# Kernel optimization log

Hardware: AMD Instinct MI355X
Metric: run time of the kernel (lower is better)

Reference implementation:

```python
import jax, jax.numpy as jnp
import numpy as np

RES = 128          # voxel grid resolution
N = 262144
C_IN = 64
C_OUT = 64
K = 3              # kernel size -> 27 offsets


def _build_rulebook(coords, res, k):
    """Submanifold sparse conv rulebook (stride=1, padding=k//2).
    Returns in_idx, out_idx [K^3, N] int32 and mask [K^3, N] float32."""
    n = coords.shape[0]
    lin = (coords[:, 0] * res + coords[:, 1]) * res + coords[:, 2]
    order = np.argsort(lin)
    sorted_lin = lin[order]
    r = k // 2
    in_idx, out_idx, mask = [], [], []
    for dx in range(-r, r + 1):
        for dy in range(-r, r + 1):
            for dz in range(-r, r + 1):
                nb = coords + np.array([dx, dy, dz])
                inb = np.all((nb >= 0) & (nb < res), axis=1)
                nlin = (nb[:, 0] * res + nb[:, 1]) * res + nb[:, 2]
                pos = np.searchsorted(sorted_lin, nlin)
                pos_c = np.clip(pos, 0, n - 1)
                found = inb & (sorted_lin[pos_c] == nlin)
                in_idx.append(np.where(found, order[pos_c], 0))
                out_idx.append(np.where(found, np.arange(n), 0))
                mask.append(found.astype(np.float32))
    return (np.asarray(in_idx, np.int32), np.asarray(out_idx, np.int32),
            np.asarray(mask, np.float32))


def setup_inputs() -> dict:
    rng = np.random.default_rng(0)
    lin = rng.choice(RES ** 3, size=N, replace=False)
    coords = np.stack([lin // (RES * RES), (lin // RES) % RES, lin % RES], axis=1)
    in_idx, out_idx, mask = _build_rulebook(coords, RES, K)

    key = jax.random.key(0)
    kf, kw, kb = jax.random.split(key, 3)
    feats = jax.random.normal(kf, (N, C_IN), dtype=jnp.float32)
    weight = jax.random.normal(kw, (K ** 3, C_IN, C_OUT), dtype=jnp.float32) * 0.02
    bias = jax.random.normal(kb, (C_OUT,), dtype=jnp.float32) * 0.02
    return {
        "feats": feats,
        "weight": weight,
        "bias": bias,
        "in_idx": jnp.asarray(in_idx),
        "out_idx": jnp.asarray(out_idx),
        "mask": jnp.asarray(mask),
    }


def reference(feats, weight, bias, in_idx, out_idx, mask):
    # gather -> GEMM -> scatter per kernel offset (27 fixed offsets)
    n = feats.shape[0]
    out = jnp.tile(bias[None, :], (n, 1))  # [N, C_out]
    for k in range(weight.shape[0]):
        g = feats[in_idx[k]] * mask[k][:, None]   # [N, C_in], zeros where no pair
        out = out.at[out_idx[k]].add(g @ weight[k])  # invalid rows add zeros at row 0
    return out
```

## Files before the change

kernel.cpp:

```cpp
#include <hip/hip_runtime.h>

#define CIN  64
#define COUT 64
#define KVOL 27

typedef __attribute__((ext_vector_type(8))) short bf16x8;
typedef __attribute__((ext_vector_type(4))) float f32x4;

union U4H8 { uint4 u; bf16x8 h; };

static __device__ __forceinline__ unsigned short f2bf(float x) {
    union { float f; unsigned int u; } v; v.f = x;
    return (unsigned short)((v.u + 0x7FFFu + ((v.u >> 16) & 1u)) >> 16);
}

__global__ __launch_bounds__(256) void pack_w(const float* __restrict__ W,
                                              unsigned short* __restrict__ wf) {
    int t = blockIdx.x * 256 + threadIdx.x;
    if (t >= KVOL * 8 * 64) return;
    int lane  = t & 63;
    int frag  = (t >> 6) & 7;
    int k     = t >> 9;
    int kh    = frag >> 2, nt = frag & 3;
    int col   = nt * 16 + (lane & 15);
    int kbase = kh * 32 + (lane >> 4) * 8;
    const float* src = W + (size_t)k * (CIN * COUT) + (size_t)kbase * COUT + col;
    unsigned int pk[4];
    #pragma unroll
    for (int j = 0; j < 4; ++j) {
        unsigned int lo = f2bf(src[(2 * j) * COUT]);
        unsigned int hi = f2bf(src[(2 * j + 1) * COUT]);
        pk[j] = lo | (hi << 16);
    }
    *reinterpret_cast<uint4*>(wf + (size_t)t * 8) = make_uint4(pk[0], pk[1], pk[2], pk[3]);
}

__global__ __launch_bounds__(256) void cvt_feats(const float* __restrict__ f,
                                                 uint4* __restrict__ o, int total8) {
    int t = blockIdx.x * 256 + threadIdx.x;
    if (t < total8) {
        const float4* p = reinterpret_cast<const float4*>(f) + 2 * (size_t)t;
        float4 a = p[0], b = p[1];
        unsigned int u0 = (unsigned int)f2bf(a.x) | ((unsigned int)f2bf(a.y) << 16);
        unsigned int u1 = (unsigned int)f2bf(a.z) | ((unsigned int)f2bf(a.w) << 16);
        unsigned int u2 = (unsigned int)f2bf(b.x) | ((unsigned int)f2bf(b.y) << 16);
        unsigned int u3 = (unsigned int)f2bf(b.z) | ((unsigned int)f2bf(b.w) << 16);
        o[t] = make_uint4(u0, u1, u2, u3);
    } else if (t < total8 + 8) {
        o[t] = make_uint4(0u, 0u, 0u, 0u);
    }
}

__global__ __launch_bounds__(256) void spconv_mfma64(
    const char* __restrict__ fbf,
    const uint4* __restrict__ wf4,
    const float* __restrict__ bias,
    const int*   __restrict__ in_idx,
    const float* __restrict__ mask,
    float* __restrict__ out, int n)
{
    const int tid  = threadIdx.x;
    const int lane = tid & 63;
    const int wv   = tid >> 6;
    const int rloc = lane & 15;
    const int grp  = lane >> 4;

    const int nwg = gridDim.x;
    int bid = blockIdx.x;
    if ((nwg & 7) == 0) {
        const int chunk = nwg >> 3;
        bid = (blockIdx.x & 7) * chunk + (blockIdx.x >> 3);
    }
    const int row0 = bid * 256 + wv * 64;

    __shared__ uint4 lds_w[2][512];

    f32x4 acc[4][4];
    #pragma unroll
    for (int nt = 0; nt < 4; ++nt) {
        float b = bias[nt * 16 + rloc];
        f32x4 v = {b, b, b, b};
        acc[0][nt] = v; acc[1][nt] = v; acc[2][nt] = v; acc[3][nt] = v;
    }

    int rowt[4];
    #pragma unroll
    for (int t = 0; t < 4; ++t) rowt[t] = row0 + 16 * t + rloc;

    const unsigned zoff = (unsigned)n * 128u;

    lds_w[0][tid]       = wf4[tid];
    lds_w[0][tid + 256] = wf4[tid + 256];
    __syncthreads();

    U4H8 a[3][4][2];
    {
        int i0[4]; float m0[4];
        #pragma unroll
        for (int t = 0; t < 4; ++t) { i0[t] = in_idx[rowt[t]]; m0[t] = mask[rowt[t]]; }
        #pragma unroll
        for (int t = 0; t < 4; ++t) {
            unsigned o = (m0[t] != 0.0f) ? (unsigned)i0[t] * 128u : zoff;
            const uint4* p = reinterpret_cast<const uint4*>(fbf + o) + grp;
            a[0][t][0].u = p[0];
            a[0][t][1].u = p[4];
        }
        #pragma unroll
        for (int t = 0; t < 4; ++t) { i0[t] = in_idx[(size_t)n + rowt[t]]; m0[t] = mask[(size_t)n + rowt[t]]; }
        #pragma unroll
        for (int t = 0; t < 4; ++t) {
            unsigned o = (m0[t] != 0.0f) ? (unsigned)i0[t] * 128u : zoff;
            const uint4* p = reinterpret_cast<const uint4*>(fbf + o) + grp;
            a[1][t][0].u = p[0];
            a[1][t][1].u = p[4];
        }
    }

    int idxb[2][4]; float mskb[2][4];
    #pragma unroll
    for (int t = 0; t < 4; ++t) {
        idxb[0][t] = in_idx[(size_t)2 * n + rowt[t]];
        mskb[0][t] = mask[(size_t)2 * n + rowt[t]];
    }
    #pragma unroll
    for (int t = 0; t < 4; ++t) {
        idxb[1][t] = in_idx[(size_t)3 * n + rowt[t]];
        mskb[1][t] = mask[(size_t)3 * n + rowt[t]];
    }

    #pragma unroll
    for (int k = 0; k < KVOL; ++k) {
        const int cur  = k & 1;
        const int nxt  = cur ^ 1;
        const int cslot = k % 3;
        const int gslot = (k + 2) % 3;
        const int islot = k & 1;

        uint4 w0, w1;
        if (k + 1 < KVOL) {
            const uint4* s = wf4 + (size_t)(k + 1) * 512;
            w0 = s[tid]; w1 = s[tid + 256];
        }

        if (k + 2 < KVOL) {
            #pragma unroll
            for (int t = 0; t < 4; ++t) {
                unsigned o = (mskb[islot][t] != 0.0f) ? (unsigned)idxb[islot][t] * 128u : zoff;
                const uint4* p = reinterpret_cast<const uint4*>(fbf + o) + grp;
                a[gslot][t][0].u = p[0];
                a[gslot][t][1].u = p[4];
            }
        }

        if (k + 4 < KVOL) {
            const size_t kb = (size_t)(k + 4) * n;
            #pragma unroll
            for (int t = 0; t < 4; ++t) {
                idxb[islot][t] = in_idx[kb + rowt[t]];
                mskb[islot][t] = mask[kb + rowt[t]];
            }
        }

        __builtin_amdgcn_sched_barrier(0);

        U4H8 bf[2][4];
        #pragma unroll
        for (int kh = 0; kh < 2; ++kh)
            #pragma unroll
            for (int ntl = 0; ntl < 4; ++ntl)
                bf[kh][ntl].u = lds_w[cur][(kh * 4 + ntl) * 64 + lane];

        #pragma unroll
        for (int t = 0; t < 4; ++t)
            #pragma unroll
            for (int ntl = 0; ntl < 4; ++ntl) {
                acc[t][ntl] = __builtin_amdgcn_mfma_f32_16x16x32_bf16(a[cslot][t][0].h, bf[0][ntl].h, acc[t][ntl], 0, 0, 0);
                acc[t][ntl] = __builtin_amdgcn_mfma_f32_16x16x32_bf16(a[cslot][t][1].h, bf[1][ntl].h, acc[t][ntl], 0, 0, 0);
            }

        if (k + 1 < KVOL) {
            lds_w[nxt][tid]       = w0;
            lds_w[nxt][tid + 256] = w1;
            asm volatile("s_waitcnt lgkmcnt(0)" ::: "memory");
            __builtin_amdgcn_s_barrier();
        }
    }

    #pragma unroll
    for (int t = 0; t < 4; ++t)
        #pragma unroll
        for (int ntl = 0; ntl < 4; ++ntl)
            #pragma unroll
            for (int r = 0; r < 4; ++r) {
                int orow = row0 + 16 * t + grp * 4 + r;
                out[(size_t)orow * COUT + ntl * 16 + rloc] = acc[t][ntl][r];
            }
}

static __device__ __forceinline__ bf16x8 cvt8(float4 a, float4 b, float m) {
    bf16x8 r;
    r[0] = (short)f2bf(a.x * m); r[1] = (short)f2bf(a.y * m);
    r[2] = (short)f2bf(a.z * m); r[3] = (short)f2bf(a.w * m);
    r[4] = (short)f2bf(b.x * m); r[5] = (short)f2bf(b.y * m);
    r[6] = (short)f2bf(b.z * m); r[7] = (short)f2bf(b.w * m);
    return r;
}

__global__ __launch_bounds__(256) void spconv_mfma_f32(
    const float* __restrict__ feats,
    const unsigned short* __restrict__ wf,
    const float* __restrict__ bias,
    const int*   __restrict__ in_idx,
    const float* __restrict__ mask,
    float* __restrict__ out, int n)
{
    const int tid  = threadIdx.x;
    const int lane = tid & 63;
    const int wv   = tid >> 6;
    const int rloc = lane & 15;
    const int grp  = lane >> 4;
    const int row0 = blockIdx.x * 128 + wv * 32;

    __shared__ uint4 lds_w[2][512];

    f32x4 acc[2][4];
    #pragma unroll
    for (int nt = 0; nt < 4; ++nt) {
        float b = bias[nt * 16 + rloc];
        f32x4 v = {b, b, b, b};
        acc[0][nt] = v; acc[1][nt] = v;
    }

    const uint4* wf4 = reinterpret_cast<const uint4*>(wf);
    lds_w[0][tid]       = wf4[tid];
    lds_w[0][tid + 256] = wf4[tid + 256];
    __syncthreads();

    const int rowA = row0 + rloc;
    const int rowB = rowA + 16;

    for (int koff = 0; koff < KVOL; ++koff) {
        const int cur = koff & 1;
        uint4 w0, w1;
        const bool pf = (koff + 1 < KVOL);
        if (pf) {
            const uint4* s = wf4 + (size_t)(koff + 1) * 512;
            w0 = s[tid]; w1 = s[tid + 256];
        }

        const size_t kb = (size_t)koff * n;
        const int   idxA = in_idx[kb + rowA];
        const float mA   = mask[kb + rowA];
        const int   idxB = in_idx[kb + rowB];
        const float mB   = mask[kb + rowB];

        const float4* fA = reinterpret_cast<const float4*>(feats + (size_t)idxA * CIN + grp * 8);
        const float4* fB = reinterpret_cast<const float4*>(feats + (size_t)idxB * CIN + grp * 8);
        float4 a0 = fA[0], a1 = fA[1], a2 = fA[8], a3 = fA[9];
        float4 c0 = fB[0], c1 = fB[1], c2 = fB[8], c3 = fB[9];

        bf16x8 aA0 = cvt8(a0, a1, mA), aA1 = cvt8(a2, a3, mA);
        bf16x8 aB0 = cvt8(c0, c1, mB), aB1 = cvt8(c2, c3, mB);

        U4H8 bf[2][4];
        #pragma unroll
        for (int kh = 0; kh < 2; ++kh)
            #pragma unroll
            for (int nt = 0; nt < 4; ++nt)
                bf[kh][nt].u = lds_w[cur][(kh * 4 + nt) * 64 + lane];

        #pragma unroll
        for (int nt = 0; nt < 4; ++nt) {
            acc[0][nt] = __builtin_amdgcn_mfma_f32_16x16x32_bf16(aA0, bf[0][nt].h, acc[0][nt], 0, 0, 0);
            acc[0][nt] = __builtin_amdgcn_mfma_f32_16x16x32_bf16(aA1, bf[1][nt].h, acc[0][nt], 0, 0, 0);
            acc[1][nt] = __builtin_amdgcn_mfma_f32_16x16x32_bf16(aB0, bf[0][nt].h, acc[1][nt], 0, 0, 0);
            acc[1][nt] = __builtin_amdgcn_mfma_f32_16x16x32_bf16(aB1, bf[1][nt].h, acc[1][nt], 0, 0, 0);
        }

        if (pf) {
            lds_w[cur ^ 1][tid]       = w0;
            lds_w[cur ^ 1][tid + 256] = w1;
        }
        __syncthreads();
    }

    #pragma unroll
    for (int t = 0; t < 2; ++t)
        #pragma unroll
        for (int nt = 0; nt < 4; ++nt)
            #pragma unroll
            for (int r = 0; r < 4; ++r) {
                int orow = row0 + t * 16 + grp * 4 + r;
                out[(size_t)orow * COUT + nt * 16 + rloc] = acc[t][nt][r];
            }
}

extern "C" void kernel_launch(void* const* d_in, const int* in_sizes, int n_in,
                              void* d_out, int out_size, void* d_ws, size_t ws_size,
                              hipStream_t stream)
{
    const float* feats  = (const float*)d_in[0];
    const float* weight = (const float*)d_in[1];
    const float* bias   = (const float*)d_in[2];
    const int*   in_idx = (const int*)  d_in[3];
    const float* mask   = (const float*)d_in[5];
    float* out = (float*)d_out;

    const int n = in_sizes[0] / CIN;

    const size_t WF_BYTES  = (size_t)KVOL * 8 * 64 * 16;
    const size_t FBF_BYTES = (size_t)(n + 1) * CIN * 2;

    unsigned short* wf = (unsigned short*)d_ws;
    const int packN = KVOL * 8 * 64;
    pack_w<<<(packN + 255) / 256, 256, 0, stream>>>(weight, wf);

    if (ws_size >= WF_BYTES + FBF_BYTES) {
        char* fbf = (char*)d_ws + WF_BYTES;
        const int total8 = n * 8;
        cvt_feats<<<(total8 + 8 + 255) / 256, 256, 0, stream>>>(feats, (uint4*)fbf, total8);
        spconv_mfma64<<<n / 256, 256, 0, stream>>>(fbf, (const uint4*)wf, bias,
                                                   in_idx, mask, out, n);
    } else {
        spconv_mfma_f32<<<n / 128, 256, 0, stream>>>(feats, wf, bias,
                                                     in_idx, mask, out, n);
    }
}
```

Before: 88.25 us.

## Gather feature rows directly into LDS via global_load_lds double buffering

Replaces the register-held triple-buffered gather of bf16 feature rows with asynchronous global-to-LDS loads into two double-buffered LDS regions per wave, then reads the A fragments from LDS before the MFMAs. The aim is to cut VGPR pressure and let the gather run asynchronously beside compute. The prefetch depth drops from two offsets ahead to one, and LDS use grows to about 80KB per block, which may limit occupancy. The only wait before reading the gathered data is the existing lgkmcnt wait and barrier, which may not be enough to cover the outstanding vmcnt for these loads.

```diff
diff --git a/kernel.cpp b/kernel.cpp
--- a/kernel.cpp
+++ b/kernel.cpp
@@ -3,6 +3,9 @@
 #define CIN  64
 #define COUT 64
 #define KVOL 27
+
+#define AS1 __attribute__((address_space(1)))
+#define AS3 __attribute__((address_space(3)))
 
 typedef __attribute__((ext_vector_type(8))) short bf16x8;
 typedef __attribute__((ext_vector_type(4))) float f32x4;
@@ -51,7 +54,7 @@
     }
 }
 
-__global__ __launch_bounds__(256) void spconv_mfma64(
+__global__ __launch_bounds__(256) void spconv_glds(
     const char* __restrict__ fbf,
     const uint4* __restrict__ wf4,
     const float* __restrict__ bias,
@@ -73,7 +76,10 @@
     }
     const int row0 = bid * 256 + wv * 64;
 
-    __shared__ uint4 lds_w[2][512];
+    __shared__ uint4 wb0[512];
+    __shared__ uint4 wb1[512];
+    __shared__ uint4 ga[4 * 512];
+    __shared__ uint4 gb[4 * 512];
 
     f32x4 acc[4][4];
     #pragma unroll
@@ -89,52 +95,60 @@
 
     const unsigned zoff = (unsigned)n * 128u;
 
-    lds_w[0][tid]       = wf4[tid];
-    lds_w[0][tid + 256] = wf4[tid + 256];
-    __syncthreads();
-
-    U4H8 a[3][4][2];
-    {
-        int i0[4]; float m0[4];
-        #pragma unroll
-        for (int t = 0; t < 4; ++t) { i0[t] = in_idx[rowt[t]]; m0[t] = mask[rowt[t]]; }
-        #pragma unroll
-        for (int t = 0; t < 4; ++t) {
-            unsigned o = (m0[t] != 0.0f) ? (unsigned)i0[t] * 128u : zoff;
-            const uint4* p = reinterpret_cast<const uint4*>(fbf + o) + grp;
-            a[0][t][0].u = p[0];
-            a[0][t][1].u = p[4];
-        }
-        #pragma unroll
-        for (int t = 0; t < 4; ++t) { i0[t] = in_idx[(size_t)n + rowt[t]]; m0[t] = mask[(size_t)n + rowt[t]]; }
-        #pragma unroll
-        for (int t = 0; t < 4; ++t) {
-            unsigned o = (m0[t] != 0.0f) ? (unsigned)i0[t] * 128u : zoff;
-            const uint4* p = reinterpret_cast<const uint4*>(fbf + o) + grp;
-            a[1][t][0].u = p[0];
-            a[1][t][1].u = p[4];
-        }
-    }
+    int i0[4]; float m0[4];
+    #pragma unroll
+    for (int t = 0; t < 4; ++t) { i0[t] = in_idx[rowt[t]]; m0[t] = mask[rowt[t]]; }
 
     int idxb[2][4]; float mskb[2][4];
+    #pragma unroll
+    for (int t = 0; t < 4; ++t) {
+        idxb[1][t] = in_idx[(size_t)n + rowt[t]];
+        mskb[1][t] = mask[(size_t)n + rowt[t]];
+    }
     #pragma unroll
     for (int t = 0; t < 4; ++t) {
         idxb[0][t] = in_idx[(size_t)2 * n + rowt[t]];
         mskb[0][t] = mask[(size_t)2 * n + rowt[t]];
     }
-    #pragma unroll
-    for (int t = 0; t < 4; ++t) {
-        idxb[1][t] = in_idx[(size_t)3 * n + rowt[t]];
-        mskb[1][t] = mask[(size_t)3 * n + rowt[t]];
-    }
+
+    {
+        unsigned o[4];
+        #pragma unroll
+        for (int t = 0; t < 4; ++t)
+            o[t] = (m0[t] != 0.0f) ? (unsigned)i0[t] * 128u : zoff;
+        #pragma unroll
+        for (int j = 0; j < 8; ++j) {
+            const char* src = fbf + o[j >> 1] + grp * 16 + (j & 1) * 64;
+            __builtin_amdgcn_global_load_lds((const AS1 void*)src,
+                (AS3 void*)(ga + wv * 512 + j * 64), 16, 0, 0);
+        }
+    }
+    {
+        uint4 w0 = wf4[tid], w1 = wf4[tid + 256];
+        wb0[tid] = w0; wb0[tid + 256] = w1;
+    }
+    __syncthreads();
 
     #pragma unroll
     for (int k = 0; k < KVOL; ++k) {
-        const int cur  = k & 1;
-        const int nxt  = cur ^ 1;
-        const int cslot = k % 3;
-        const int gslot = (k + 2) % 3;
-        const int islot = k & 1;
+        uint4* wc = (k & 1) ? wb1 : wb0;
+        uint4* wn = (k & 1) ? wb0 : wb1;
+        uint4* gc = (k & 1) ? gb : ga;
+        uint4* gn = (k & 1) ? ga : gb;
+
+        if (k + 1 < KVOL) {
+            const int p = (k + 1) & 1;
+            unsigned o[4];
+            #pragma unroll
+            for (int t = 0; t < 4; ++t)
+                o[t] = (mskb[p][t] != 0.0f) ? (unsigned)idxb[p][t] * 128u : zoff;
+            #pragma unroll
+            for (int j = 0; j < 8; ++j) {
+                const char* src = fbf + o[j >> 1] + grp * 16 + (j & 1) * 64;
+                __builtin_amdgcn_global_load_lds((const AS1 void*)src,
+                    (AS3 void*)(gn + wv * 512 + j * 64), 16, 0, 0);
+            }
+        }
 
         uint4 w0, w1;
         if (k + 1 < KVOL) {
@@ -142,22 +156,13 @@
             w0 = s[tid]; w1 = s[tid + 256];
         }
 
-        if (k + 2 < KVOL) {
+        if (k + 3 < KVOL) {
+            const int p = (k + 1) & 1;
+            const size_t kb = (size_t)(k + 3) * n;
             #pragma unroll
             for (int t = 0; t < 4; ++t) {
-                unsigned o = (mskb[islot][t] != 0.0f) ? (unsigned)idxb[islot][t] * 128u : zoff;
-                const uint4* p = reinterpret_cast<const uint4*>(fbf + o) + grp;
-                a[gslot][t][0].u = p[0];
-                a[gslot][t][1].u = p[4];
-            }
-        }
-
-        if (k + 4 < KVOL) {
-            const size_t kb = (size_t)(k + 4) * n;
-            #pragma unroll
-            for (int t = 0; t < 4; ++t) {
-                idxb[islot][t] = in_idx[kb + rowt[t]];
-                mskb[islot][t] = mask[kb + rowt[t]];
+                idxb[p][t] = in_idx[kb + rowt[t]];
+                mskb[p][t] = mask[kb + rowt[t]];
             }
         }
 
@@ -168,19 +173,24 @@
         for (int kh = 0; kh < 2; ++kh)
             #pragma unroll
             for (int ntl = 0; ntl < 4; ++ntl)
-                bf[kh][ntl].u = lds_w[cur][(kh * 4 + ntl) * 64 + lane];
+                bf[kh][ntl].u = wc[(kh * 4 + ntl) * 64 + lane];
+
+        U4H8 af[4][2];
+        #pragma unroll
+        for (int j = 0; j < 8; ++j)
+            af[j >> 1][j & 1].u = gc[wv * 512 + j * 64 + lane];
 
         #pragma unroll
         for (int t = 0; t < 4; ++t)
             #pragma unroll
             for (int ntl = 0; ntl < 4; ++ntl) {
-                acc[t][ntl] = __builtin_amdgcn_mfma_f32_16x16x32_bf16(a[cslot][t][0].h, bf[0][ntl].h, acc[t][ntl], 0, 0, 0);
-                acc[t][ntl] = __builtin_amdgcn_mfma_f32_16x16x32_bf16(a[cslot][t][1].h, bf[1][ntl].h, acc[t][ntl], 0, 0, 0);
+                acc[t][ntl] = __builtin_amdgcn_mfma_f32_16x16x32_bf16(af[t][0].h, bf[0][ntl].h, acc[t][ntl], 0, 0, 0);
+                acc[t][ntl] = __builtin_amdgcn_mfma_f32_16x16x32_bf16(af[t][1].h, bf[1][ntl].h, acc[t][ntl], 0, 0, 0);
             }
 
         if (k + 1 < KVOL) {
-            lds_w[nxt][tid]       = w0;
-            lds_w[nxt][tid + 256] = w1;
+            wn[tid]       = w0;
+            wn[tid + 256] = w1;
             asm volatile("s_waitcnt lgkmcnt(0)" ::: "memory");
             __builtin_amdgcn_s_barrier();
         }
@@ -319,8 +329,8 @@
         char* fbf = (char*)d_ws + WF_BYTES;
         const int total8 = n * 8;
         cvt_feats<<<(total8 + 8 + 255) / 256, 256, 0, stream>>>(feats, (uint4*)fbf, total8);
-        spconv_mfma64<<<n / 256, 256, 0, stream>>>(fbf, (const uint4*)wf, bias,
-                                                   in_idx, mask, out, n);
+        spconv_glds<<<n / 256, 256, 0, stream>>>(fbf, (const uint4*)wf, bias,
+                                                 in_idx, mask, out, n);
     } else {
         spconv_mfma_f32<<<n / 128, 256, 0, stream>>>(feats, wf, bias,
                                                      in_idx, mask, out, n);
```

Result: slower. 91.17 us (+3.3%).

## Process kernel offsets in pairs to halve barriers and deepen prefetch

Applied to the files above, without the earlier changes.

Restructures the main loop to handle two kernel offsets per iteration. Weights for both offsets are double-buffered in LDS, and gathered features and indices are prefetched a pair ahead. This halves the number of block-wide barriers and LDS weight-swap phases, and puts more independent gathers in flight per step. The cost is more registers (the feature buffer grows from 3x to 4x row slots, plus extra index staging) and double the LDS, which may lower occupancy.

```diff
diff --git a/kernel.cpp b/kernel.cpp
--- a/kernel.cpp
+++ b/kernel.cpp
@@ -51,7 +51,7 @@
     }
 }
 
-__global__ __launch_bounds__(256) void spconv_mfma64(
+__global__ __launch_bounds__(256) void spconv_pair(
     const char* __restrict__ fbf,
     const uint4* __restrict__ wf4,
     const float* __restrict__ bias,
@@ -73,7 +73,7 @@
     }
     const int row0 = bid * 256 + wv * 64;
 
-    __shared__ uint4 lds_w[2][512];
+    __shared__ uint4 lds_w[2][2][512];
 
     f32x4 acc[4][4];
     #pragma unroll
@@ -89,101 +89,135 @@
 
     const unsigned zoff = (unsigned)n * 128u;
 
-    lds_w[0][tid]       = wf4[tid];
-    lds_w[0][tid + 256] = wf4[tid + 256];
+    int ia[4], ib[4]; float ma[4], mb[4];
+    #pragma unroll
+    for (int t = 0; t < 4; ++t) { ia[t] = in_idx[rowt[t]];              ma[t] = mask[rowt[t]]; }
+    #pragma unroll
+    for (int t = 0; t < 4; ++t) { ib[t] = in_idx[(size_t)n + rowt[t]];  mb[t] = mask[(size_t)n + rowt[t]]; }
+
+    {
+        uint4 w0 = wf4[tid], w1 = wf4[tid + 256];
+        uint4 w2 = wf4[512 + tid], w3 = wf4[512 + tid + 256];
+        lds_w[0][0][tid] = w0; lds_w[0][0][tid + 256] = w1;
+        lds_w[0][1][tid] = w2; lds_w[0][1][tid + 256] = w3;
+    }
     __syncthreads();
 
-    U4H8 a[3][4][2];
-    {
-        int i0[4]; float m0[4];
-        #pragma unroll
-        for (int t = 0; t < 4; ++t) { i0[t] = in_idx[rowt[t]]; m0[t] = mask[rowt[t]]; }
+    U4H8 a[2][2][4][2];
+    #pragma unroll
+    for (int t = 0; t < 4; ++t) {
+        unsigned o = (ma[t] != 0.0f) ? (unsigned)ia[t] * 128u : zoff;
+        const uint4* p = reinterpret_cast<const uint4*>(fbf + o) + grp;
+        a[0][0][t][0].u = p[0]; a[0][0][t][1].u = p[4];
+    }
+    #pragma unroll
+    for (int t = 0; t < 4; ++t) {
+        unsigned o = (mb[t] != 0.0f) ? (unsigned)ib[t] * 128u : zoff;
+        const uint4* p = reinterpret_cast<const uint4*>(fbf + o) + grp;
+        a[0][1][t][0].u = p[0]; a[0][1][t][1].u = p[4];
+    }
+
+    int idxb[2][2][4]; float mskb[2][2][4];
+    #pragma unroll
+    for (int ks = 0; ks < 2; ++ks)
         #pragma unroll
         for (int t = 0; t < 4; ++t) {
-            unsigned o = (m0[t] != 0.0f) ? (unsigned)i0[t] * 128u : zoff;
-            const uint4* p = reinterpret_cast<const uint4*>(fbf + o) + grp;
-            a[0][t][0].u = p[0];
-            a[0][t][1].u = p[4];
-        }
-        #pragma unroll
-        for (int t = 0; t < 4; ++t) { i0[t] = in_idx[(size_t)n + rowt[t]]; m0[t] = mask[(size_t)n + rowt[t]]; }
+            idxb[1][ks][t] = in_idx[(size_t)(2 + ks) * n + rowt[t]];
+            mskb[1][ks][t] = mask[(size_t)(2 + ks) * n + rowt[t]];
+        }
+    #pragma unroll
+    for (int ks = 0; ks < 2; ++ks)
         #pragma unroll
         for (int t = 0; t < 4; ++t) {
-            unsigned o = (m0[t] != 0.0f) ? (unsigned)i0[t] * 128u : zoff;
-            const uint4* p = reinterpret_cast<const uint4*>(fbf + o) + grp;
-            a[1][t][0].u = p[0];
-            a[1][t][1].u = p[4];
-        }
-    }
-
-    int idxb[2][4]; float mskb[2][4];
-    #pragma unroll
-    for (int t = 0; t < 4; ++t) {
-        idxb[0][t] = in_idx[(size_t)2 * n + rowt[t]];
-        mskb[0][t] = mask[(size_t)2 * n + rowt[t]];
-    }
-    #pragma unroll
-    for (int t = 0; t < 4; ++t) {
-        idxb[1][t] = in_idx[(size_t)3 * n + rowt[t]];
-        mskb[1][t] = mask[(size_t)3 * n + rowt[t]];
-    }
-
-    #pragma unroll
-    for (int k = 0; k < KVOL; ++k) {
-        const int cur  = k & 1;
-        const int nxt  = cur ^ 1;
-        const int cslot = k % 3;
-        const int gslot = (k + 2) % 3;
-        const int islot = k & 1;
-
-        uint4 w0, w1;
-        if (k + 1 < KVOL) {
-            const uint4* s = wf4 + (size_t)(k + 1) * 512;
+            idxb[0][ks][t] = in_idx[(size_t)(4 + ks) * n + rowt[t]];
+            mskb[0][ks][t] = mask[(size_t)(4 + ks) * n + rowt[t]];
+        }
+
+    #pragma unroll
+    for (int p = 0; p < 14; ++p) {
+        const int cur = p & 1;
+        const int nxt = cur ^ 1;
+        const int k0 = 2 * p;
+        const int k1 = 2 * p + 1;
+
+        uint4 w0, w1, w2, w3;
+        if (2 * p + 2 < KVOL) {
+            const uint4* s = wf4 + (size_t)(2 * p + 2) * 512;
             w0 = s[tid]; w1 = s[tid + 256];
         }
-
-        if (k + 2 < KVOL) {
-            #pragma unroll
-            for (int t = 0; t < 4; ++t) {
-                unsigned o = (mskb[islot][t] != 0.0f) ? (unsigned)idxb[islot][t] * 128u : zoff;
-                const uint4* p = reinterpret_cast<const uint4*>(fbf + o) + grp;
-                a[gslot][t][0].u = p[0];
-                a[gslot][t][1].u = p[4];
+        if (2 * p + 3 < KVOL) {
+            const uint4* s = wf4 + (size_t)(2 * p + 3) * 512;
+            w2 = s[tid]; w3 = s[tid + 256];
+        }
+
+        #pragma unroll
+        for (int ks = 0; ks < 2; ++ks) {
+            if (2 * (p + 1) + ks < KVOL) {
+                #pragma unroll
+                for (int t = 0; t < 4; ++t) {
+                    unsigned o = (mskb[nxt][ks][t] != 0.0f)
+                               ? (unsigned)idxb[nxt][ks][t] * 128u : zoff;
+                    const uint4* q = reinterpret_cast<const uint4*>(fbf + o) + grp;
+                    a[nxt][ks][t][0].u = q[0];
+                    a[nxt][ks][t][1].u = q[4];
+                }
             }
         }
 
-        if (k + 4 < KVOL) {
-            const size_t kb = (size_t)(k + 4) * n;
-            #pragma unroll
-            for (int t = 0; t < 4; ++t) {
-                idxb[islot][t] = in_idx[kb + rowt[t]];
-                mskb[islot][t] = mask[kb + rowt[t]];
+        #pragma unroll
+        for (int ks = 0; ks < 2; ++ks) {
+            if (2 * (p + 3) + ks < KVOL) {
+                const size_t kb = (size_t)(2 * (p + 3) + ks) * n;
+                #pragma unroll
+                for (int t = 0; t < 4; ++t) {
+                    idxb[nxt][ks][t] = in_idx[kb + rowt[t]];
+                    mskb[nxt][ks][t] = mask[kb + rowt[t]];
+                }
             }
         }
 
         __builtin_amdgcn_sched_barrier(0);
 
-        U4H8 bf[2][4];
-        #pragma unroll
-        for (int kh = 0; kh < 2; ++kh)
-            #pragma unroll
-            for (int ntl = 0; ntl < 4; ++ntl)
-                bf[kh][ntl].u = lds_w[cur][(kh * 4 + ntl) * 64 + lane];
-
-        #pragma unroll
-        for (int t = 0; t < 4; ++t)
-            #pragma unroll
-            for (int ntl = 0; ntl < 4; ++ntl) {
-                acc[t][ntl] = __builtin_amdgcn_mfma_f32_16x16x32_bf16(a[cslot][t][0].h, bf[0][ntl].h, acc[t][ntl], 0, 0, 0);
-                acc[t][ntl] = __builtin_amdgcn_mfma_f32_16x16x32_bf16(a[cslot][t][1].h, bf[1][ntl].h, acc[t][ntl], 0, 0, 0);
-            }
-
-        if (k + 1 < KVOL) {
-            lds_w[nxt][tid]       = w0;
-            lds_w[nxt][tid + 256] = w1;
+        {
+            U4H8 bf[2][4];
+            #pragma unroll
+            for (int kh = 0; kh < 2; ++kh)
+                #pragma unroll
+                for (int ntl = 0; ntl < 4; ++ntl)
+                    bf[kh][ntl].u = lds_w[cur][0][(kh * 4 + ntl) * 64 + lane];
+            #pragma unroll
+            for (int t = 0; t < 4; ++t)
+                #pragma unroll
+                for (int ntl = 0; ntl < 4; ++ntl) {
+                    acc[t][ntl] = __builtin_amdgcn_mfma_f32_16x16x32_bf16(a[cur][0][t][0].h, bf[0][ntl].h, acc[t][ntl], 0, 0, 0);
+                    acc[t][ntl] = __builtin_amdgcn_mfma_f32_16x16x32_bf16(a[cur][0][t][1].h, bf[1][ntl].h, acc[t][ntl], 0, 0, 0);
+                }
+        }
+
+        if (k1 < KVOL) {
+            U4H8 bf[2][4];
+            #pragma unroll
+            for (int kh = 0; kh < 2; ++kh)
+                #pragma unroll
+                for (int ntl = 0; ntl < 4; ++ntl)
+                    bf[kh][ntl].u = lds_w[cur][1][(kh * 4 + ntl) * 64 + lane];
+            #pragma unroll
+            for (int t = 0; t < 4; ++t)
+                #pragma unroll
+                for (int ntl = 0; ntl < 4; ++ntl) {
+                    acc[t][ntl] = __builtin_amdgcn_mfma_f32_16x16x32_bf16(a[cur][1][t][0].h, bf[0][ntl].h, acc[t][ntl], 0, 0, 0);
+                    acc[t][ntl] = __builtin_amdgcn_mfma_f32_16x16x32_bf16(a[cur][1][t][1].h, bf[1][ntl].h, acc[t][ntl], 0, 0, 0);
+                }
+        }
+
+        if (p + 1 < 14) {
+            if (2 * p + 2 < KVOL) { lds_w[nxt][0][tid] = w0; lds_w[nxt][0][tid + 256] = w1; }
+            if (2 * p + 3 < KVOL) { lds_w[nxt][1][tid] = w2; lds_w[nxt][1][tid + 256] = w3; }
             asm volatile("s_waitcnt lgkmcnt(0)" ::: "memory");
             __builtin_amdgcn_s_barrier();
         }
+
+        (void)k0;
     }
 
     #pragma unroll
@@ -319,8 +353,8 @@
         char* fbf = (char*)d_ws + WF_BYTES;
         const int total8 = n * 8;
         cvt_feats<<<(total8 + 8 + 255) / 256, 256, 0, stream>>>(feats, (uint4*)fbf, total8);
-        spconv_mfma64<<<n / 256, 256, 0, stream>>>(fbf, (const uint4*)wf, bias,
-                                                   in_idx, mask, out, n);
+        spconv_pair<<<n / 256, 256, 0, stream>>>(fbf, (const uint4*)wf, bias,
+                                                 in_idx, mask, out, n);
     } else {
         spconv_mfma_f32<<<n / 128, 256, 0, stream>>>(feats, wf, bias,
                                                      in_idx, mask, out, n);
```

Result: slower. 98.98 us (+12.2%).
